# Kernel tuning notes

Hardware: AMD Instinct MI355X
Metric: run time of the kernel (lower is better)

Reference implementation:

```python
import jax, jax.numpy as jnp
from jax import lax
import numpy as np

C = 256       # residual_channels == skip_channels
B = 4
T = 4096
LATENT = 128
NB = 4        # n_blocks
NL = 10       # n_layers
ENC_DILS = tuple(2 ** i for i in range(NL)) * NB   # 40 encoder blocks
DEC_DILS = tuple(2 ** i for i in range(NL))        # 10 decoder blocks


def causal_conv(x, W, b, d):
    # x: [B, Cin, T], W: [Cout, Cin, k], left-pad by (k-1)*d for causality
    pad = (W.shape[-1] - 1) * d
    y = lax.conv_general_dilated(x, W, (1,), [(pad, 0)], rhs_dilation=(d,),
                                 dimension_numbers=('NCH', 'OIH', 'NCH'))
    return y + b[None, :, None]


def gated_block(h, Wf, bf, Wg, bg, Wr, br, Ws, bs, d):
    f = jnp.tanh(causal_conv(h, Wf, bf, d))
    g = jax.nn.sigmoid(causal_conv(h, Wg, bg, d))
    out = f * g
    res = jnp.einsum('oc,bct->bot', Wr, out) + br[None, :, None] + h
    skip = jnp.einsum('oc,bct->bot', Ws, out) + bs[None, :, None]
    return res, skip


def setup_inputs() -> dict:
    key = jax.random.key(0)
    ks = jax.random.split(key, 24)
    s = 0.05
    nE = NB * NL
    d = {}
    d['x'] = jax.random.normal(ks[0], (B, 1, T), jnp.float32)
    d['eps'] = jax.random.normal(ks[1], (B, LATENT), jnp.float32)
    d['enc_in_W'] = jax.random.normal(ks[2], (C, 1, 2)) * s
    d['enc_in_b'] = jnp.zeros((C,), jnp.float32)
    d['enc_Wf'] = jax.random.normal(ks[3], (nE, C, C, 2)) * s
    d['enc_bf'] = jnp.zeros((nE, C), jnp.float32)
    d['enc_Wg'] = jax.random.normal(ks[4], (nE, C, C, 2)) * s
    d['enc_bg'] = jnp.zeros((nE, C), jnp.float32)
    d['enc_Wr'] = jax.random.normal(ks[5], (nE, C, C)) * s
    d['enc_br'] = jnp.zeros((nE, C), jnp.float32)
    d['enc_Ws'] = jax.random.normal(ks[6], (nE, C, C)) * s
    d['enc_bs'] = jnp.zeros((nE, C), jnp.float32)
    d['fc_mu_W'] = jax.random.normal(ks[7], (LATENT, C)) * s
    d['fc_mu_b'] = jnp.zeros((LATENT,), jnp.float32)
    d['fc_lv_W'] = jax.random.normal(ks[8], (LATENT, C)) * s
    d['fc_lv_b'] = jnp.zeros((LATENT,), jnp.float32)
    d['dec_in_W'] = jax.random.normal(ks[9], (C, LATENT)) * s
    d['dec_in_b'] = jnp.zeros((C,), jnp.float32)
    d['dec_Wf'] = jax.random.normal(ks[10], (NL, C, C, 2)) * s
    d['dec_bf'] = jnp.zeros((NL, C), jnp.float32)
    d['dec_Wg'] = jax.random.normal(ks[11], (NL, C, C, 2)) * s
    d['dec_bg'] = jnp.zeros((NL, C), jnp.float32)
    d['dec_Wr'] = jax.random.normal(ks[12], (NL, C, C)) * s
    d['dec_br'] = jnp.zeros((NL, C), jnp.float32)
    d['out_W'] = jax.random.normal(ks[13], (1, C)) * s
    d['out_b'] = jnp.zeros((1,), jnp.float32)
    return d


def _forward(x, eps, enc_in_W, enc_in_b, enc_Wf, enc_bf, enc_Wg, enc_bg,
             enc_Wr, enc_br, enc_Ws, enc_bs, fc_mu_W, fc_mu_b, fc_lv_W, fc_lv_b,
             dec_in_W, dec_in_b, dec_Wf, dec_bf, dec_Wg, dec_bg, dec_Wr, dec_br,
             out_W, out_b):
    # --- encode ---
    h = causal_conv(x, enc_in_W, enc_in_b, 1)
    skip_sum = jnp.zeros((h.shape[0], C, h.shape[2]), h.dtype)
    for i, dil in enumerate(ENC_DILS):
        h, skip = gated_block(h, enc_Wf[i], enc_bf[i], enc_Wg[i], enc_bg[i],
                              enc_Wr[i], enc_br[i], enc_Ws[i], enc_bs[i], dil)
        skip_sum = skip_sum + skip
    pooled = skip_sum.mean(axis=-1)                      # [B, C]
    mu = pooled @ fc_mu_W.T + fc_mu_b                    # [B, LATENT]
    logvar = pooled @ fc_lv_W.T + fc_lv_b
    # --- reparameterize ---
    z = mu + eps * jnp.exp(0.5 * logvar)
    # --- decode (length-1 sequence) ---
    h2 = (jnp.einsum('ol,bl->bo', dec_in_W, z) + dec_in_b)[:, :, None]  # [B, C, 1]
    for i, dil in enumerate(DEC_DILS):
        f = jnp.tanh(causal_conv(h2, dec_Wf[i], dec_bf[i], dil))
        g = jax.nn.sigmoid(causal_conv(h2, dec_Wg[i], dec_bg[i], dil))
        out = f * g
        h2 = jnp.einsum('oc,bct->bot', dec_Wr[i], out) + dec_br[i][None, :, None] + h2
    y = jnp.einsum('oc,bct->bot', out_W, h2) + out_b[None, :, None]     # [B, 1, 1]
    return (y, mu, logvar)


def reference(x, eps, enc_in_W, enc_in_b, enc_Wf, enc_bf, enc_Wg, enc_bg,
              enc_Wr, enc_br, enc_Ws, enc_bs, fc_mu_W, fc_mu_b, fc_lv_W, fc_lv_b,
              dec_in_W, dec_in_b, dec_Wf, dec_bf, dec_Wg, dec_bg, dec_Wr, dec_br,
              out_W, out_b):
    return _forward(x, eps, enc_in_W, enc_in_b, enc_Wf, enc_bf, enc_Wg, enc_bg,
                    enc_Wr, enc_br, enc_Ws, enc_bs, fc_mu_W, fc_mu_b, fc_lv_W, fc_lv_b,
                    dec_in_W, dec_in_b, dec_Wf, dec_bf, dec_Wg, dec_bg, dec_Wr, dec_br,
                    out_W, out_b)
```

## Files before the change

### kernel.cpp

```cpp
#include <hip/hip_runtime.h>

typedef unsigned short u16;
typedef __attribute__((ext_vector_type(8))) __bf16 bf16x8;
typedef __attribute__((ext_vector_type(4))) float f32x4;

constexpr int C = 256;
constexpr int T = 4096;
constexpr int B = 4;
constexpr int NENC = 40;
constexpr int NDEC = 10;
constexpr int TILE = 64;

__device__ __forceinline__ float bf2f(u16 v) {
  union { unsigned u; float f; } x;
  x.u = ((unsigned)v) << 16;
  return x.f;
}
__device__ __forceinline__ u16 f2bf(float f) {
  union { float ff; unsigned u; } x;
  x.ff = f;
  unsigned r = x.u + 0x7fffu + ((x.u >> 16) & 1u);
  return (u16)(r >> 16);
}
__device__ __forceinline__ int swz(int row, int col) {
  int g = ((row & 7) ^ (row >> 3)) & 7;
  return row * 512 + (col ^ (g << 3));
}

typedef __attribute__((address_space(1))) const unsigned int* gp1_t;
typedef __attribute__((address_space(3))) unsigned int* lp3_t;
__device__ __forceinline__ void gl_lds16(const u16* g, u16* l) {
  __builtin_amdgcn_global_load_lds((gp1_t)(const void*)g, (lp3_t)(void*)l, 16, 0, 0);
}

__global__ void k_pack1(const float* __restrict__ Wf, const float* __restrict__ Wg,
                        u16* __restrict__ penc1, int total) {
  int p = blockIdx.x * 256 + threadIdx.x;
  if (p >= total) return;
  int lane = p & 63;
  int s = (p >> 6) & 3;
  int c = (p >> 8) & 15;
  int wv = (p >> 12) & 7;
  int layer = p >> 15;
  int co = wv * 32 + (s & 1) * 16 + (lane & 15);
  int k = c * 32 + (lane >> 4) * 8;
  const float* src = (s >= 2 ? Wg : Wf) + ((size_t)layer * C + co) * 512 + k;
  u16* dst = penc1 + (size_t)p * 8;
#pragma unroll
  for (int r = 0; r < 8; ++r) dst[r] = f2bf(src[r]);
}

__global__ void k_pack2(const float* __restrict__ Wr, u16* __restrict__ penc2, int total) {
  int p = blockIdx.x * 256 + threadIdx.x;
  if (p >= total) return;
  int lane = p & 63;
  int s = (p >> 6) & 1;
  int c = (p >> 7) & 7;
  int wv = (p >> 10) & 7;
  int layer = p >> 13;
  int co = wv * 32 + s * 16 + (lane & 15);
  int k = c * 32 + (lane >> 4) * 8;
  const float* src = Wr + ((size_t)layer * C + co) * 256 + k;
  u16* dst = penc2 + (size_t)p * 8;
#pragma unroll
  for (int r = 0; r < 8; ++r) dst[r] = f2bf(src[r]);
}

__global__ void k_packd(const float* __restrict__ dWf, const float* __restrict__ dWg,
                        const float* __restrict__ dWr, const float* __restrict__ dinW,
                        u16* __restrict__ pdfg, u16* __restrict__ pdr,
                        u16* __restrict__ tdin) {
  int p = blockIdx.x * 256 + threadIdx.x;
  if (p < 163840) {
    int lane = p & 63;
    int s = (p >> 6) & 1;
    int c = (p >> 7) & 7;
    int wv = (p >> 10) & 15;
    int layer = p >> 14;
    int co = wv * 16 + (lane & 15);
    int k = c * 32 + (lane >> 4) * 8;
    const float* src = (s ? dWg : dWf) + (((size_t)(layer * C + co)) * C + k) * 2 + 1;
    u16* dst = pdfg + (size_t)p * 8;
#pragma unroll
    for (int r = 0; r < 8; ++r) dst[r] = f2bf(src[2 * r]);
  } else if (p < 245760) {
    int q = p - 163840;
    int lane = q & 63;
    int c = (q >> 6) & 7;
    int wv = (q >> 9) & 15;
    int layer = q >> 13;
    int co = wv * 16 + (lane & 15);
    int k = c * 32 + (lane >> 4) * 8;
    const float* src = dWr + ((size_t)(layer * C + co)) * C + k;
    u16* dst = pdr + (size_t)q * 8;
#pragma unroll
    for (int r = 0; r < 8; ++r) dst[r] = f2bf(src[r]);
  } else if (p < 249856) {
    int u = p - 245760;
#pragma unroll
    for (int r = 0; r < 8; ++r) tdin[u * 8 + r] = f2bf(dinW[u * 8 + r]);
  }
}

__global__ void k_zero(float* __restrict__ p, int n) {
  int i = blockIdx.x * 256 + threadIdx.x;
  if (i < n) p[i] = 0.f;
}

__global__ void k_input(const float* __restrict__ x, const float* __restrict__ W,
                        const float* __restrict__ bin, float* __restrict__ h) {
  int idx = blockIdx.x * 256 + threadIdx.x;
  int t = idx & (T - 1);
  int c = (idx >> 12) & (C - 1);
  int b = idx >> 20;
  float xv = x[b * T + t];
  float xp = (t > 0) ? x[b * T + t - 1] : 0.f;
  h[idx] = W[2 * c] * xp + W[2 * c + 1] * xv + bin[c];
}

__global__ __launch_bounds__(512, 2) void k_enc(
    const float* __restrict__ hin, float* __restrict__ hout, float* __restrict__ rowsum_l,
    const u16* __restrict__ pw1, const float* __restrict__ bfb,
    const float* __restrict__ bgb,
    const u16* __restrict__ pw2, const float* __restrict__ brb,
    int dil) {
  extern __shared__ __align__(16) u16 smem[];
  u16* wb = smem + 64 * 512;
  const int tid = threadIdx.x;
  const int wave = tid >> 6;
  const int lane = tid & 63;
  const int ncol = lane & 15;
  const int quad = lane >> 4;
  const int wg = blockIdx.x;
  const int b = wg >> 6;
  const int t0 = (wg & 63) * TILE;
  const float* hb = hin + b * C * T;

  const int co0 = wave * 32;
  const int kq = quad * 8;
  const u16* b1 = pw1 + wave * 32768 + lane * 8;
  const u16* b2 = pw2 + wave * 8192 + lane * 8;
  u16* wreg0 = wb + wave * 2048;
  u16* wreg1 = wb + 16384 + wave * 2048;
  const int aoff = lane * 8;

#pragma unroll
  for (int cc = 0; cc < 2; ++cc) {
    u16* ld = cc ? wreg1 : wreg0;
    gl_lds16(b1 + cc * 2048, ld);
    gl_lds16(b1 + cc * 2048 + 512, ld + 512);
    gl_lds16(b1 + cc * 2048 + 1024, ld + 1024);
    gl_lds16(b1 + cc * 2048 + 1536, ld + 1536);
  }

  const int n4 = tid & 15;
  const int cib = tid >> 4;
  float4 v[16];
  const bool fast0 = ((dil & 3) == 0) && (t0 >= dil);
  if (fast0) {
#pragma unroll
    for (int it2 = 0; it2 < 16; ++it2) {
      int ci = (cib + it2 * 32) & 255;
      int tap = it2 >> 3;
      int tb = t0 + n4 * 4 - (tap ? 0 : dil);
      v[it2] = *(const float4*)(hb + ci * T + tb);
    }
  } else {
#pragma unroll
    for (int it2 = 0; it2 < 16; ++it2) {
      int ci = (cib + it2 * 32) & 255;
      int tap = it2 >> 3;
      int tb = t0 + n4 * 4 - (tap ? 0 : dil);
      const float* p = hb + ci * T + tb;
      if (tap) {
        v[it2] = *(const float4*)p;
      } else {
        v[it2].x = (tb + 0 >= 0) ? p[0] : 0.f;
        v[it2].y = (tb + 1 >= 0) ? p[1] : 0.f;
        v[it2].z = (tb + 2 >= 0) ? p[2] : 0.f;
        v[it2].w = (tb + 3 >= 0) ? p[3] : 0.f;
      }
    }
  }
#pragma unroll
  for (int it2 = 0; it2 < 8; ++it2) {
    int ci = (cib + it2 * 32) & 255;
    const float* p0 = (const float*)&v[it2];
    const float* p1 = (const float*)&v[it2 + 8];
#pragma unroll
    for (int r = 0; r < 4; ++r) {
      unsigned w32 = (unsigned)f2bf(p0[r]) | ((unsigned)f2bf(p1[r]) << 16);
      *(unsigned*)(&smem[swz(n4 * 4 + r, 2 * ci)]) = w32;
    }
  }
  __syncthreads();

  f32x4 acc[4][4];
#pragma unroll
  for (int m = 0; m < 4; ++m)
#pragma unroll
    for (int nt = 0; nt < 4; ++nt)
      acc[m][nt] = (f32x4){0.f, 0.f, 0.f, 0.f};

#pragma unroll
  for (int c = 0; c < 16; ++c) {
    if (c < 15) asm volatile("s_waitcnt vmcnt(4)" ::: "memory");
    else        asm volatile("s_waitcnt vmcnt(0)" ::: "memory");
    const u16* wr_ = (c & 1) ? wreg1 : wreg0;
    bf16x8 af0 = *(const bf16x8*)(wr_ + aoff);
    bf16x8 af1 = *(const bf16x8*)(wr_ + 512 + aoff);
    bf16x8 af2 = *(const bf16x8*)(wr_ + 1024 + aoff);
    bf16x8 af3 = *(const bf16x8*)(wr_ + 1536 + aoff);
    const int kk = c * 32 + kq;
    bf16x8 bfr[4];
#pragma unroll
    for (int nt = 0; nt < 4; ++nt)
      bfr[nt] = *(const bf16x8*)(&smem[swz(nt * 16 + ncol, kk)]);
#pragma unroll
    for (int nt = 0; nt < 4; ++nt) {
      acc[0][nt] = __builtin_amdgcn_mfma_f32_16x16x32_bf16(af0, bfr[nt], acc[0][nt], 0, 0, 0);
      acc[1][nt] = __builtin_amdgcn_mfma_f32_16x16x32_bf16(af1, bfr[nt], acc[1][nt], 0, 0, 0);
      acc[2][nt] = __builtin_amdgcn_mfma_f32_16x16x32_bf16(af2, bfr[nt], acc[2][nt], 0, 0, 0);
      acc[3][nt] = __builtin_amdgcn_mfma_f32_16x16x32_bf16(af3, bfr[nt], acc[3][nt], 0, 0, 0);
    }
    if (c + 2 < 16) {
      asm volatile("s_waitcnt lgkmcnt(0)" ::: "memory");
      u16* ld = (c & 1) ? wreg1 : wreg0;
      const u16* gs = b1 + (c + 2) * 2048;
      gl_lds16(gs, ld);
      gl_lds16(gs + 512, ld + 512);
      gl_lds16(gs + 1024, ld + 1024);
      gl_lds16(gs + 1536, ld + 1536);
    }
  }

#pragma unroll
  for (int cc = 0; cc < 2; ++cc) {
    u16* ld = cc ? wreg1 : wreg0;
    gl_lds16(b2 + cc * 1024, ld);
    gl_lds16(b2 + cc * 1024 + 512, ld + 512);
  }
  __syncthreads();

  float* rsb = rowsum_l + b * C;
#pragma unroll
  for (int j = 0; j < 2; ++j) {
    const int cob = co0 + j * 16 + quad * 4;
    float bfv[4], bgv[4], rs[4];
#pragma unroll
    for (int r = 0; r < 4; ++r) {
      bfv[r] = bfb[cob + r];
      bgv[r] = bgb[cob + r];
      rs[r] = 0.f;
    }
#pragma unroll
    for (int nt = 0; nt < 4; ++nt) {
      const int n = nt * 16 + ncol;
      u16 pk[4];
#pragma unroll
      for (int r = 0; r < 4; ++r) {
        float fv = acc[j][nt][r] + bfv[r];
        float gv = acc[2 + j][nt][r] + bgv[r];
        float th = 1.f - 2.f / (__expf(2.f * fv) + 1.f);
        float sg = 1.f / (1.f + __expf(-gv));
        float o = th * sg;
        rs[r] += o;
        pk[r] = f2bf(o);
      }
      uint2 w;
      w.x = (unsigned)pk[0] | ((unsigned)pk[1] << 16);
      w.y = (unsigned)pk[2] | ((unsigned)pk[3] << 16);
      *(uint2*)(&smem[swz(n, cob)]) = w;
    }
#pragma unroll
    for (int r = 0; r < 4; ++r) {
      float s = rs[r];
      s += __shfl_xor(s, 1);
      s += __shfl_xor(s, 2);
      s += __shfl_xor(s, 4);
      s += __shfl_xor(s, 8);
      if (ncol == 0) atomicAdd(&rsb[cob + r], s);
    }
  }
  __syncthreads();

  f32x4 acc2[2][4];
#pragma unroll
  for (int m = 0; m < 2; ++m)
#pragma unroll
    for (int nt = 0; nt < 4; ++nt)
      acc2[m][nt] = (f32x4){0.f, 0.f, 0.f, 0.f};

#pragma unroll
  for (int c = 0; c < 8; ++c) {
    if (c < 7) asm volatile("s_waitcnt vmcnt(2)" ::: "memory");
    else       asm volatile("s_waitcnt vmcnt(0)" ::: "memory");
    const u16* wr_ = (c & 1) ? wreg1 : wreg0;
    bf16x8 af0 = *(const bf16x8*)(wr_ + aoff);
    bf16x8 af1 = *(const bf16x8*)(wr_ + 512 + aoff);
    const int kk = c * 32 + kq;
    bf16x8 bfr[4];
#pragma unroll
    for (int nt = 0; nt < 4; ++nt)
      bfr[nt] = *(const bf16x8*)(&smem[swz(nt * 16 + ncol, kk)]);
#pragma unroll
    for (int nt = 0; nt < 4; ++nt) {
      acc2[0][nt] = __builtin_amdgcn_mfma_f32_16x16x32_bf16(af0, bfr[nt], acc2[0][nt], 0, 0, 0);
      acc2[1][nt] = __builtin_amdgcn_mfma_f32_16x16x32_bf16(af1, bfr[nt], acc2[1][nt], 0, 0, 0);
    }
    if (c + 2 < 8) {
      asm volatile("s_waitcnt lgkmcnt(0)" ::: "memory");
      u16* ld = (c & 1) ? wreg1 : wreg0;
      const u16* gs = b2 + (c + 2) * 1024;
      gl_lds16(gs, ld);
      gl_lds16(gs + 512, ld + 512);
    }
  }

  float hold[32];
  float brv[2][4];
#pragma unroll
  for (int m = 0; m < 2; ++m)
#pragma unroll
    for (int r = 0; r < 4; ++r)
      brv[m][r] = brb[co0 + m * 16 + quad * 4 + r];
#pragma unroll
  for (int m = 0; m < 2; ++m)
#pragma unroll
    for (int nt = 0; nt < 4; ++nt)
#pragma unroll
      for (int r = 0; r < 4; ++r)
        hold[(m * 4 + nt) * 4 + r] =
            hb[(co0 + m * 16 + quad * 4 + r) * T + (t0 + nt * 16 + ncol)];

  float* ho = hout + b * C * T;
#pragma unroll
  for (int m = 0; m < 2; ++m)
#pragma unroll
    for (int nt = 0; nt < 4; ++nt)
#pragma unroll
      for (int r = 0; r < 4; ++r)
        ho[(co0 + m * 16 + quad * 4 + r) * T + (t0 + nt * 16 + ncol)] =
            acc2[m][nt][r] + brv[m][r] + hold[(m * 4 + nt) * 4 + r];
}

__global__ __launch_bounds__(256) void k_skip(
    const float* __restrict__ encWs, const float* __restrict__ encbs,
    const float* __restrict__ rowsum, float* __restrict__ pooled) {
  __shared__ float rs[B][C];
  const int l = blockIdx.x;
  const int co = threadIdx.x;
  for (int i = co; i < B * C; i += 256) rs[i >> 8][i & 255] = rowsum[l * B * C + i];
  __syncthreads();
  const float* Wrow = encWs + (size_t)l * C * C + co * C;
  float bs = encbs[l * C + co] * (float)T;
  float d[B] = {0.f, 0.f, 0.f, 0.f};
  for (int ci = 0; ci < C; ci += 4) {
    float4 w = *(const float4*)(Wrow + ci);
#pragma unroll
    for (int b = 0; b < B; ++b)
      d[b] += w.x * rs[b][ci] + w.y * rs[b][ci + 1] + w.z * rs[b][ci + 2] + w.w * rs[b][ci + 3];
  }
#pragma unroll
  for (int b = 0; b < B; ++b) atomicAdd(&pooled[b * C + co], d[b] + bs);
}

__global__ __launch_bounds__(256) void k_fc(
    const float* __restrict__ pooled,
    const float* __restrict__ muW, const float* __restrict__ mub,
    const float* __restrict__ lvW, const float* __restrict__ lvb,
    float* __restrict__ mlbuf, float* __restrict__ dout) {
  __shared__ float pm[B * C];
  const int tid = threadIdx.x;
  for (int i = tid; i < B * C; i += 256) pm[i] = pooled[i] * (1.f / (float)T);
  __syncthreads();
  const int waveG = blockIdx.x * 4 + (tid >> 6);
  const int lane = tid & 63;
  for (int j = 0; j < 16; ++j) {
    int d = waveG * 16 + j;
    int b = d >> 8, r = d & 255, which = r >> 7, l = r & 127;
    const float* Wrow = (which ? lvW : muW) + l * C;
    const float* p = pm + b * C;
    float s = Wrow[lane] * p[lane] + Wrow[lane + 64] * p[lane + 64] +
              Wrow[lane + 128] * p[lane + 128] + Wrow[lane + 192] * p[lane + 192];
#pragma unroll
    for (int off = 32; off; off >>= 1) s += __shfl_xor(s, off);
    if (lane == 0) {
      float val = s + (which ? lvb[l] : mub[l]);
      mlbuf[which * 512 + b * 128 + l] = val;
      dout[4 + which * 512 + b * 128 + l] = val;
    }
  }
}

__global__ __launch_bounds__(1024, 1) void k_dec(
    const float* __restrict__ mlbuf, const float* __restrict__ eps,
    const u16* __restrict__ tdin, const float* __restrict__ dinb,
    const u16* __restrict__ pdfg, const float* __restrict__ dbf,
    const float* __restrict__ dbg,
    const u16* __restrict__ pdr, const float* __restrict__ dbr,
    const float* __restrict__ outW, const float* __restrict__ outb,
    float* __restrict__ dout) {
  extern __shared__ __align__(16) u16 dsm[];
  __shared__ __align__(16) u16 Ah[16][264];
  __shared__ __align__(16) u16 Ao[16][264];
  __shared__ float h2f[4][256];
  __shared__ float outred[4];
  const int tid = threadIdx.x;
  const int wave = tid >> 6;
  const int lane = tid & 63;
  const int ncol = lane & 15;
  const int quad = lane >> 4;
  const int kq = quad * 8;
  const int co = wave * 16 + ncol;
  u16* wreg = dsm + wave * 4096;

  bf16x8 tdw[4];
  {
    const u16* wp = tdin + co * 128;
#pragma unroll
    for (int it = 0; it < 4; ++it) tdw[it] = *(const bf16x8*)(wp + it * 32 + kq);
  }

  if (tid < 512) {
    int b = tid >> 7, l = tid & 127;
    float mu = mlbuf[b * 128 + l];
    float lv = mlbuf[512 + b * 128 + l];
    Ah[b][l] = f2bf(mu + eps[b * 128 + l] * expf(0.5f * lv));
  }
  if (tid < 4) outred[tid] = 0.f;
  __syncthreads();

  {
    f32x4 acch = (f32x4){0.f, 0.f, 0.f, 0.f};
#pragma unroll
    for (int it = 0; it < 4; ++it) {
      bf16x8 af = *(const bf16x8*)(&Ah[ncol][it * 32 + kq]);
      acch = __builtin_amdgcn_mfma_f32_16x16x32_bf16(af, tdw[it], acch, 0, 0, 0);
    }
    __syncthreads();
    if (quad == 0) {
      float bias = dinb[co];
#pragma unroll
      for (int r = 0; r < 4; ++r) {
        float hv = acch[r] + bias;
        h2f[r][co] = hv;
        Ah[r][co] = f2bf(hv);
      }
    }
  }
  {
    const u16* fb = pdfg + wave * 8192 + lane * 8;
#pragma unroll
    for (int cc = 0; cc < 4; ++cc) {
      gl_lds16(fb + cc * 1024, wreg + cc * 1024);
      gl_lds16(fb + cc * 1024 + 512, wreg + cc * 1024 + 512);
    }
  }
  __syncthreads();

  for (int i = 0; i < NDEC; ++i) {
    const u16* fb = pdfg + (i * 16 + wave) * 8192 + lane * 8;
    const u16* rb = pdr + (i * 16 + wave) * 4096 + lane * 8;

    f32x4 accf = (f32x4){0.f, 0.f, 0.f, 0.f};
    f32x4 accg = (f32x4){0.f, 0.f, 0.f, 0.f};
#pragma unroll
    for (int c = 0; c < 8; ++c) {
      if (c == 4) asm volatile("s_waitcnt vmcnt(6)" ::: "memory");
      else if (c == 5) asm volatile("s_waitcnt vmcnt(4)" ::: "memory");
      else if (c == 6) asm volatile("s_waitcnt vmcnt(2)" ::: "memory");
      else if (c == 7) asm volatile("s_waitcnt vmcnt(0)" ::: "memory");
      const u16* bufp = wreg + (c & 3) * 1024;
      bf16x8 bf_ = *(const bf16x8*)(bufp + lane * 8);
      bf16x8 bg_ = *(const bf16x8*)(bufp + 512 + lane * 8);
      bf16x8 af = *(const bf16x8*)(&Ah[ncol][c * 32 + kq]);
      accf = __builtin_amdgcn_mfma_f32_16x16x32_bf16(af, bf_, accf, 0, 0, 0);
      accg = __builtin_amdgcn_mfma_f32_16x16x32_bf16(af, bg_, accg, 0, 0, 0);
      if (c < 4) {
        asm volatile("s_waitcnt lgkmcnt(0)" ::: "memory");
        gl_lds16(fb + (c + 4) * 1024, wreg + (c & 3) * 1024);
        gl_lds16(fb + (c + 4) * 1024 + 512, wreg + (c & 3) * 1024 + 512);
      }
    }
    asm volatile("s_waitcnt lgkmcnt(0)" ::: "memory");
#pragma unroll
    for (int cc = 0; cc < 4; ++cc) gl_lds16(rb + cc * 512, wreg + cc * 1024);

    if (quad == 0) {
      float bfv = dbf[i * C + co];
      float bgv = dbg[i * C + co];
#pragma unroll
      for (int r = 0; r < 4; ++r) {
        float fv = accf[r] + bfv;
        float gv = accg[r] + bgv;
        float th = 1.f - 2.f / (__expf(2.f * fv) + 1.f);
        float sg = 1.f / (1.f + __expf(-gv));
        Ao[r][co] = f2bf(th * sg);
      }
    }
    __syncthreads();

    f32x4 accr = (f32x4){0.f, 0.f, 0.f, 0.f};
#pragma unroll
    for (int c = 0; c < 8; ++c) {
      if (c == 4) asm volatile("s_waitcnt vmcnt(3)" ::: "memory");
      else if (c == 5) asm volatile("s_waitcnt vmcnt(2)" ::: "memory");
      else if (c == 6) asm volatile("s_waitcnt vmcnt(1)" ::: "memory");
      else if (c == 7) asm volatile("s_waitcnt vmcnt(0)" ::: "memory");
      bf16x8 br_ = *(const bf16x8*)(wreg + (c & 3) * 1024 + lane * 8);
      bf16x8 af = *(const bf16x8*)(&Ao[ncol][c * 32 + kq]);
      accr = __builtin_amdgcn_mfma_f32_16x16x32_bf16(af, br_, accr, 0, 0, 0);
      if (c < 4) {
        asm volatile("s_waitcnt lgkmcnt(0)" ::: "memory");
        gl_lds16(rb + (c + 4) * 512, wreg + (c & 3) * 1024);
      }
    }
    if (i + 1 < NDEC) {
      const u16* nfb = pdfg + ((i + 1) * 16 + wave) * 8192 + lane * 8;
      asm volatile("s_waitcnt lgkmcnt(0)" ::: "memory");
#pragma unroll
      for (int cc = 0; cc < 4; ++cc) {
        gl_lds16(nfb + cc * 1024, wreg + cc * 1024);
        gl_lds16(nfb + cc * 1024 + 512, wreg + cc * 1024 + 512);
      }
    }
    if (quad == 0) {
      float brv = dbr[i * C + co];
#pragma unroll
      for (int r = 0; r < 4; ++r) {
        float hv = h2f[r][co] + accr[r] + brv;
        h2f[r][co] = hv;
        Ah[r][co] = f2bf(hv);
      }
    }
    __syncthreads();
  }

  {
    int b = tid >> 8, c = tid & 255;
    float val = outW[c] * h2f[b][c];
#pragma unroll
    for (int off = 32; off; off >>= 1) val += __shfl_xor(val, off);
    if (lane == 0) atomicAdd(&outred[b], val);
  }
  __syncthreads();
  if (tid < 4) dout[tid] = outred[tid] + outb[0];
}

extern "C" void kernel_launch(void* const* d_in, const int* in_sizes, int n_in,
                              void* d_out, int out_size, void* d_ws, size_t ws_size,
                              hipStream_t stream) {
  const float* x      = (const float*)d_in[0];
  const float* eps    = (const float*)d_in[1];
  const float* encinW = (const float*)d_in[2];
  const float* encinb = (const float*)d_in[3];
  const float* encWf  = (const float*)d_in[4];
  const float* encbf  = (const float*)d_in[5];
  const float* encWg  = (const float*)d_in[6];
  const float* encbg  = (const float*)d_in[7];
  const float* encWr  = (const float*)d_in[8];
  const float* encbr  = (const float*)d_in[9];
  const float* encWs  = (const float*)d_in[10];
  const float* encbs  = (const float*)d_in[11];
  const float* muW    = (const float*)d_in[12];
  const float* mub    = (const float*)d_in[13];
  const float* lvW    = (const float*)d_in[14];
  const float* lvb    = (const float*)d_in[15];
  const float* dinW   = (const float*)d_in[16];
  const float* dinb   = (const float*)d_in[17];
  const float* dWf    = (const float*)d_in[18];
  const float* dbf    = (const float*)d_in[19];
  const float* dWg    = (const float*)d_in[20];
  const float* dbg    = (const float*)d_in[21];
  const float* dWr    = (const float*)d_in[22];
  const float* dbr    = (const float*)d_in[23];
  const float* outW   = (const float*)d_in[24];
  const float* outb   = (const float*)d_in[25];
  float* dout = (float*)d_out;

  char* ws = (char*)d_ws;
  float* hA = (float*)ws;
  float* hB = hA + (size_t)B * C * T;
  float* pooled = hB + (size_t)B * C * T;
  float* mlbuf = pooled + B * C;
  float* rowsum = mlbuf + 1024;
  u16* penc1 = (u16*)(rowsum + NENC * B * C);
  u16* penc2 = penc1 + (size_t)10485760;
  u16* pdfg = penc2 + (size_t)2621440;
  u16* pdr = pdfg + (size_t)1310720;
  u16* tdin = pdr + (size_t)655360;

  (void)hipFuncSetAttribute(reinterpret_cast<const void*>(k_enc),
                            hipFuncAttributeMaxDynamicSharedMemorySize, 131072);
  (void)hipFuncSetAttribute(reinterpret_cast<const void*>(k_dec),
                            hipFuncAttributeMaxDynamicSharedMemorySize, 131072);

  k_pack1<<<(1310720 + 255) / 256, 256, 0, stream>>>(encWf, encWg, penc1, 1310720);
  k_pack2<<<(327680 + 255) / 256, 256, 0, stream>>>(encWr, penc2, 327680);
  k_packd<<<(249856 + 255) / 256, 256, 0, stream>>>(dWf, dWg, dWr, dinW, pdfg, pdr, tdin);

  const int nZ = B * C + 1024 + NENC * B * C;
  k_zero<<<(nZ + 255) / 256, 256, 0, stream>>>(pooled, nZ);
  k_input<<<(B * C * T) / 256, 256, 0, stream>>>(x, encinW, encinb, hA);

  for (int i = 0; i < NENC; ++i) {
    const int dil = 1 << (i % 10);
    const float* hi = (i & 1) ? hB : hA;
    float* ho = (i & 1) ? hA : hB;
    k_enc<<<256, 512, 131072, stream>>>(
        hi, ho, rowsum + (size_t)i * B * C,
        penc1 + (size_t)i * 262144, encbf + (size_t)i * C,
        encbg + (size_t)i * C,
        penc2 + (size_t)i * 65536, encbr + (size_t)i * C,
        dil);
  }

  k_skip<<<NENC, 256, 0, stream>>>(encWs, encbs, rowsum, pooled);
  k_fc<<<16, 256, 0, stream>>>(pooled, muW, mub, lvW, lvb, mlbuf, dout);
  k_dec<<<1, 1024, 131072, stream>>>(mlbuf, eps, tdin, dinb, pdfg, dbf, dbg,
                                     pdr, dbr, outW, outb, dout);
}
```

Before: 1.324 ms.

## Reuse loaded tap-1 inputs for residual and stage output through LDS for coalesced stores

The epilogue no longer re-reads the residual input h from global memory. It reuses the current-tap values already held in registers from the input load. Accumulators plus bias are staged through shared memory with a padded stride, so each thread writes coalesced float4 rows instead of strided scalar stores. The input-load fast path now also covers unaligned dilations by splitting the tap-0 load into scalar reads. This adds two block barriers and keeps the v registers live longer, which raises register pressure.

```diff
diff --git a/kernel.cpp b/kernel.cpp
--- a/kernel.cpp
+++ b/kernel.cpp
@@ -156,14 +156,19 @@
   const int n4 = tid & 15;
   const int cib = tid >> 4;
   float4 v[16];
-  const bool fast0 = ((dil & 3) == 0) && (t0 >= dil);
-  if (fast0) {
+  const bool al4 = ((dil & 3) == 0);
+  if (t0 >= dil) {
 #pragma unroll
     for (int it2 = 0; it2 < 16; ++it2) {
       int ci = (cib + it2 * 32) & 255;
       int tap = it2 >> 3;
       int tb = t0 + n4 * 4 - (tap ? 0 : dil);
-      v[it2] = *(const float4*)(hb + ci * T + tb);
+      const float* p = hb + ci * T + tb;
+      if (tap || al4) {
+        v[it2] = *(const float4*)p;
+      } else {
+        v[it2].x = p[0]; v[it2].y = p[1]; v[it2].z = p[2]; v[it2].w = p[3];
+      }
     }
   } else {
 #pragma unroll
@@ -316,32 +321,33 @@
       gl_lds16(gs + 512, ld + 512);
     }
   }
-
-  float hold[32];
-  float brv[2][4];
-#pragma unroll
-  for (int m = 0; m < 2; ++m)
-#pragma unroll
-    for (int r = 0; r < 4; ++r)
-      brv[m][r] = brb[co0 + m * 16 + quad * 4 + r];
-#pragma unroll
-  for (int m = 0; m < 2; ++m)
-#pragma unroll
-    for (int nt = 0; nt < 4; ++nt)
+  __syncthreads();
+
+  float* fb = (float*)smem;
+#pragma unroll
+  for (int m = 0; m < 2; ++m) {
+    const int cob = co0 + m * 16 + quad * 4;
+#pragma unroll
+    for (int nt = 0; nt < 4; ++nt) {
+      const int t = nt * 16 + ncol;
 #pragma unroll
       for (int r = 0; r < 4; ++r)
-        hold[(m * 4 + nt) * 4 + r] =
-            hb[(co0 + m * 16 + quad * 4 + r) * T + (t0 + nt * 16 + ncol)];
-
+        fb[(cob + r) * 66 + t] = acc2[m][nt][r] + brb[cob + r];
+    }
+  }
+  __syncthreads();
   float* ho = hout + b * C * T;
 #pragma unroll
-  for (int m = 0; m < 2; ++m)
-#pragma unroll
-    for (int nt = 0; nt < 4; ++nt)
-#pragma unroll
-      for (int r = 0; r < 4; ++r)
-        ho[(co0 + m * 16 + quad * 4 + r) * T + (t0 + nt * 16 + ncol)] =
-            acc2[m][nt][r] + brv[m][r] + hold[(m * 4 + nt) * 4 + r];
+  for (int it2 = 0; it2 < 8; ++it2) {
+    const int ci = cib + it2 * 32;
+    const float* fr = fb + ci * 66 + n4 * 4;
+    float4 o;
+    o.x = fr[0] + v[it2 + 8].x;
+    o.y = fr[1] + v[it2 + 8].y;
+    o.z = fr[2] + v[it2 + 8].z;
+    o.w = fr[3] + v[it2 + 8].w;
+    *(float4*)(ho + ci * T + t0 + n4 * 4) = o;
+  }
 }
 
 __global__ __launch_bounds__(256) void k_skip(
```

New measurement: 1.279 ms. 1.04x faster.
